# Performance work log

Measured on AMD Instinct MI355X. Metric: run time of the kernel, lower is better.

Reference implementation:

```python
import jax, jax.numpy as jnp
import numpy as np

V, E, H, S, B, T = 32000, 256, 512, 128, 32, 32


def setup_inputs() -> dict:
    key = jax.random.key(0)
    ks = iter(jax.random.split(key, 32))

    def w(shape, s=0.05):
        return jax.random.normal(next(ks), shape, dtype=jnp.float32) * s

    return dict(
        src=jax.random.randint(next(ks), (S, B), 0, V),
        trg=jax.random.randint(next(ks), (T, B), 0, V),
        embed=w((V, E)),
        enc_Wih_f=w((4 * H, E)), enc_Whh_f=w((4 * H, H)), enc_bih_f=w((4 * H,)), enc_bhh_f=w((4 * H,)),
        enc_Wih_b=w((4 * H, E)), enc_Whh_b=w((4 * H, H)), enc_bih_b=w((4 * H,)), enc_bhh_b=w((4 * H,)),
        attn_W=w((H, 2 * H)), attn_b=w((H,)), attn_v=w((H,)),
        dec_Wih0=w((4 * H, H + E)), dec_Whh0=w((4 * H, H)), dec_bih0=w((4 * H,)), dec_bhh0=w((4 * H,)),
        dec_Wih1=w((4 * H, H)), dec_Whh1=w((4 * H, H)), dec_bih1=w((4 * H,)), dec_bhh1=w((4 * H,)),
        out_W=w((V, 2 * H)), out_b=w((V,)),
    )


def _cell(x, h, c, Wih, Whh, bih, bhh):
    # PyTorch LSTM gate order: i, f, g, o
    z = x @ Wih.T + h @ Whh.T + bih + bhh
    i, f, g, o = jnp.split(z, 4, axis=-1)
    c2 = jax.nn.sigmoid(f) * c + jax.nn.sigmoid(i) * jnp.tanh(g)
    h2 = jax.nn.sigmoid(o) * jnp.tanh(c2)
    return h2, c2


def _run_lstm(xs, Wih, Whh, bih, bhh):
    # xs: [S, B, in]; returns outputs [S,B,H], final (h,c)
    h0 = jnp.zeros((xs.shape[1], Whh.shape[1]), xs.dtype)

    def step(carry, x):
        h, c = carry
        h2, c2 = _cell(x, h, c, Wih, Whh, bih, bhh)
        return (h2, c2), h2

    (hT, cT), outs = jax.lax.scan(step, (h0, h0), xs)
    return outs, hT, cT


def _forward(src, trg, embed,
             enc_Wih_f, enc_Whh_f, enc_bih_f, enc_bhh_f,
             enc_Wih_b, enc_Whh_b, enc_bih_b, enc_bhh_b,
             attn_W, attn_b, attn_v,
             dec_Wih0, dec_Whh0, dec_bih0, dec_bhh0,
             dec_Wih1, dec_Whh1, dec_bih1, dec_bhh1,
             out_W, out_b):
    emb_src = embed[src]                                  # [S,B,E]
    # bidirectional 1-layer encoder LSTM
    f_outs, hf, cf = _run_lstm(emb_src, enc_Wih_f, enc_Whh_f, enc_bih_f, enc_bhh_f)
    b_outs, hb, cb = _run_lstm(emb_src[::-1], enc_Wih_b, enc_Whh_b, enc_bih_b, enc_bhh_b)
    enc_out = f_outs + b_outs[::-1]                       # [S,B,H] (sum of directions)
    h = jnp.stack([hf, hb])                               # [2,B,H] -> decoder init state
    c = jnp.stack([cf, cb])
    enc_bsh = enc_out.transpose(1, 0, 2)                  # [B,S,H]

    def dec_step(carry, tok):
        h, c = carry
        emb = embed[tok]                                  # [B,E]
        q = h[-1]                                         # top-layer hidden [B,H]
        qs = jnp.broadcast_to(q[:, None, :], enc_bsh.shape)
        energy = jnp.tanh(jnp.concatenate([qs, enc_bsh], -1) @ attn_W.T + attn_b)  # [B,S,H]
        scores = energy @ attn_v                          # [B,S]
        aw = jax.nn.softmax(scores, axis=1)
        ctx = jnp.einsum('bs,bsh->bh', aw, enc_bsh)       # [B,H]
        x = jnp.concatenate([emb, ctx], -1)               # [B,E+H]
        h0, c0 = _cell(x, h[0], c[0], dec_Wih0, dec_Whh0, dec_bih0, dec_bhh0)
        h1, c1 = _cell(h0, h[1], c[1], dec_Wih1, dec_Whh1, dec_bih1, dec_bhh1)
        logits = jax.nn.log_softmax(
            jnp.concatenate([h1, ctx], -1) @ out_W.T + out_b, axis=-1)             # [B,V]
        return (jnp.stack([h0, h1]), jnp.stack([c0, c1])), logits

    # teacher forcing (ratio=1.0): input at step t is trg[t-1]
    _, outs = jax.lax.scan(dec_step, (h, c), trg[:-1])    # [T-1,B,V]
    outputs = jnp.concatenate(
        [jnp.zeros((1,) + outs.shape[1:], outs.dtype), outs], 0)  # outputs[0]=0 as in torch
    return outputs


def reference(src, trg, embed,
              enc_Wih_f, enc_Whh_f, enc_bih_f, enc_bhh_f,
              enc_Wih_b, enc_Whh_b, enc_bih_b, enc_bhh_b,
              attn_W, attn_b, attn_v,
              dec_Wih0, dec_Whh0, dec_bih0, dec_bhh0,
              dec_Wih1, dec_Whh1, dec_bih1, dec_bhh1,
              out_W, out_b):
    return _forward(src, trg, embed,
                    enc_Wih_f, enc_Whh_f, enc_bih_f, enc_bhh_f,
                    enc_Wih_b, enc_Whh_b, enc_bih_b, enc_bhh_b,
                    attn_W, attn_b, attn_v,
                    dec_Wih0, dec_Whh0, dec_bih0, dec_bhh0,
                    dec_Wih1, dec_Whh1, dec_bih1, dec_bhh1,
                    out_W, out_b)
```

## Files before the change

### kernel.cpp

```cpp
#include <hip/hip_runtime.h>
#include <stdint.h>


using short8 = __attribute__((ext_vector_type(8))) short;
using f32x4  = __attribute__((ext_vector_type(4))) float;
typedef _Float16 half2v __attribute__((ext_vector_type(2)));

__device__ __forceinline__ short f2bf(float x){
  unsigned u = __float_as_uint(x);
  unsigned r = (u + 0x7fffu + ((u >> 16) & 1u)) >> 16;
  return (short)(unsigned short)r;
}
__device__ __forceinline__ float bf2f_lo(unsigned u){ return __uint_as_float(u << 16); }
__device__ __forceinline__ float bf2f_hi(unsigned u){ return __uint_as_float(u & 0xffff0000u); }
__device__ __forceinline__ float sigmf(float x){ return 1.0f/(1.0f + __expf(-x)); }
__device__ __forceinline__ float fast_tanh(float x){
  const float e = __expf(2.0f*x);
  return 1.0f - 2.0f/(e + 1.0f);
}
__device__ __forceinline__ unsigned pack_h2(float a, float b){
  unsigned short ha = __builtin_bit_cast(unsigned short, (_Float16)a);
  unsigned short hb = __builtin_bit_cast(unsigned short, (_Float16)b);
  return (unsigned)ha | ((unsigned)hb << 16);
}
__device__ __forceinline__ float h2lo(unsigned u){ return (float)__builtin_bit_cast(half2v,u)[0]; }
__device__ __forceinline__ float h2hi(unsigned u){ return (float)__builtin_bit_cast(half2v,u)[1]; }
__device__ __forceinline__ float dot2u(unsigned x, unsigned w, float c){
#if __has_builtin(__builtin_amdgcn_fdot2)
  return __builtin_amdgcn_fdot2(__builtin_bit_cast(half2v,x), __builtin_bit_cast(half2v,w), c, false);
#else
  half2v hx = __builtin_bit_cast(half2v,x), hw = __builtin_bit_cast(half2v,w);
  c = fmaf((float)hx[0], (float)hw[0], c);
  c = fmaf((float)hx[1], (float)hw[1], c);
  return c;
#endif
}

__device__ __forceinline__ float4 load_coh_f4(const float* p){
  float4 v;
  asm volatile("global_load_dwordx4 %0, %1, off sc0 sc1\n\ts_waitcnt vmcnt(0)"
               : "=&v"(v) : "v"(p) : "memory");
  return v;
}
__device__ __forceinline__ void store_coh_u32(unsigned* p, unsigned v){
  asm volatile("global_store_dword %0, %1, off sc0 sc1" :: "v"(p), "v"(v) : "memory");
}

__device__ __forceinline__ void wait_spread(const unsigned* base, int n, unsigned target){
  if (threadIdx.x < 64){
    const bool mine = (int)threadIdx.x < n;
    const unsigned* p = base + (threadIdx.x << 4);
    for(;;){
      unsigned v = target;
      if (mine)
        asm volatile("global_load_dword %0, %1, off sc0 sc1\n\ts_waitcnt vmcnt(0)"
                     : "=&v"(v) : "v"(p) : "memory");
      if (__all(v >= target)) break;
    }
  }
  __syncthreads();
}
__device__ __forceinline__ void set_flag_sp(unsigned* slot, unsigned val){
  asm volatile("s_waitcnt vmcnt(0)" ::: "memory");
  __syncthreads();
  if (threadIdx.x == 0) store_coh_u32(slot, val);
}

__device__ __forceinline__ void stage8u(const unsigned* src, int bg, unsigned* lds){
  const unsigned* s0 = src + (size_t)bg*2048;
  const int f0 = threadIdx.x, f1 = f0 + 256;
  uint4 a, b;
  asm volatile(
    "global_load_dwordx4 %0, %2, off sc0 sc1\n\t"
    "global_load_dwordx4 %1, %3, off sc0 sc1\n\t"
    "s_waitcnt vmcnt(0)"
    : "=&v"(a), "=&v"(b)
    : "v"(s0 + (f0<<2)), "v"(s0 + (f1<<2))
    : "memory");
  { const int row = f0>>6, cu = (f0&63)<<2; *(uint4*)&lds[row*260+cu] = a; }
  { const int row = f1>>6, cu = (f1&63)<<2; *(uint4*)&lds[row*260+cu] = b; }
}

__device__ __forceinline__ float dot512(const unsigned* xrow, const unsigned* w){
  float a = 0.f;
  #pragma unroll 4
  for (int it = 0; it < 16; ++it){
    uint4 x0 = *(const uint4*)(xrow + it*16);
    uint4 x1 = *(const uint4*)(xrow + it*16 + 4);
    uint4 x2 = *(const uint4*)(xrow + it*16 + 8);
    uint4 x3 = *(const uint4*)(xrow + it*16 + 12);
    uint4 w0 = *(const uint4*)(w + it*16);
    uint4 w1 = *(const uint4*)(w + it*16 + 4);
    uint4 w2 = *(const uint4*)(w + it*16 + 8);
    uint4 w3 = *(const uint4*)(w + it*16 + 12);
    a = dot2u(x0.x,w0.x,a); a = dot2u(x0.y,w0.y,a); a = dot2u(x0.z,w0.z,a); a = dot2u(x0.w,w0.w,a);
    a = dot2u(x1.x,w1.x,a); a = dot2u(x1.y,w1.y,a); a = dot2u(x1.z,w1.z,a); a = dot2u(x1.w,w1.w,a);
    a = dot2u(x2.x,w2.x,a); a = dot2u(x2.y,w2.y,a); a = dot2u(x2.z,w2.z,a); a = dot2u(x2.w,w2.w,a);
    a = dot2u(x3.x,w3.x,a); a = dot2u(x3.y,w3.y,a); a = dot2u(x3.z,w3.z,a); a = dot2u(x3.w,w3.w,a);
  }
  return a;
}

__device__ __forceinline__ float2 dot2rows(const unsigned* xrow, const unsigned* wA, const unsigned* wB){
  float a = 0.f, b = 0.f;
  #pragma unroll 8
  for (int it = 0; it < 32; ++it){
    uint4 x0 = *(const uint4*)(xrow + it*8);
    uint4 x1 = *(const uint4*)(xrow + it*8 + 4);
    uint4 a0 = *(const uint4*)(wA + it*8);
    uint4 a1 = *(const uint4*)(wA + it*8 + 4);
    uint4 b0 = *(const uint4*)(wB + it*8);
    uint4 b1 = *(const uint4*)(wB + it*8 + 4);
    a = dot2u(x0.x,a0.x,a); a = dot2u(x0.y,a0.y,a); a = dot2u(x0.z,a0.z,a); a = dot2u(x0.w,a0.w,a);
    a = dot2u(x1.x,a1.x,a); a = dot2u(x1.y,a1.y,a); a = dot2u(x1.z,a1.z,a); a = dot2u(x1.w,a1.w,a);
    b = dot2u(x0.x,b0.x,b); b = dot2u(x0.y,b0.y,b); b = dot2u(x0.z,b0.z,b); b = dot2u(x0.w,b0.w,b);
    b = dot2u(x1.x,b1.x,b); b = dot2u(x1.y,b1.y,b); b = dot2u(x1.z,b1.z,b); b = dot2u(x1.w,b1.w,b);
  }
  return make_float2(a, b);
}

__global__ void k_zero(float* __restrict__ p, int n){
  int i = blockIdx.x*256 + threadIdx.x;
  const int stride = gridDim.x*256;
  for (; i < n; i += stride) p[i] = 0.f;
}

__global__ __launch_bounds__(256) void k_cvt_f16(const float* __restrict__ s, unsigned short* __restrict__ d, int n){
  int i = blockIdx.x*256 + threadIdx.x;
  const int stride = gridDim.x*256;
  for (; i < n; i += stride) d[i] = __builtin_bit_cast(unsigned short, (_Float16)s[i]);
}
__global__ __launch_bounds__(256) void k_cvt_f16_str(const float* __restrict__ s, int lds_, unsigned short* __restrict__ d, int n){
  int i = blockIdx.x*256 + threadIdx.x;
  const int stride = gridDim.x*256;
  for (; i < n; i += stride){
    const int row = i >> 9, c = i & 511;
    d[i] = __builtin_bit_cast(unsigned short, (_Float16)s[(size_t)row*lds_ + c]);
  }
}

__global__ __launch_bounds__(256) void k_gather(
    const int* __restrict__ src, const int* __restrict__ trg,
    const float* __restrict__ embed,
    short* __restrict__ emb_src_bf, short* __restrict__ emb_trg_bf)
{
  const int row = blockIdx.x, tid = threadIdx.x;
  if (row < 4096){
    const int tok = src[row];
    emb_src_bf[(size_t)row*256 + tid] = f2bf(embed[(size_t)tok*256 + tid]);
  } else {
    const int r = row - 4096;
    short v = 0;
    if (r < 992){ const int tok = trg[r]; v = f2bf(embed[(size_t)tok*256 + tid]); }
    emb_trg_bf[(size_t)r*256 + tid] = v;
  }
}

__global__ __launch_bounds__(256) void k_gemm_aw(
    const short* __restrict__ A, int lda,
    const float* __restrict__ W, int ldw,
    float* __restrict__ C, int ldc,
    const float* __restrict__ bias0, const float* __restrict__ bias1,
    int Mvalid, int K, int tmode, short* __restrict__ Cbf)
{
  __shared__ __align__(16) short As[128*32];
  __shared__ __align__(16) short Bs[128*32];
  const int tid = threadIdx.x;
  const int bm = blockIdx.x, bn = blockIdx.y;
  const int w  = tid >> 6,  l  = tid & 63;
  const int wm = w >> 1,    wn = w & 1;
  const int lr = l & 15,    lk = l >> 4;

  const int r0 = tid >> 2;
  const int s0 = (tid & 3) << 3;
  const int r1 = r0 + 64;

  const short* a0 = A + (size_t)(bm*128 + r0)*lda + s0;
  const short* a1 = A + (size_t)(bm*128 + r1)*lda + s0;
  const float* w0 = W + (size_t)(bn*128 + r0)*ldw + s0;
  const float* w1 = W + (size_t)(bn*128 + r1)*ldw + s0;

  const f32x4 zero4 = {0.f,0.f,0.f,0.f};
  f32x4 acc[4][4];
  #pragma unroll
  for (int mi=0;mi<4;mi++){
    #pragma unroll
    for (int ni=0;ni<4;ni++) acc[mi][ni] = zero4;
  }

  for (int k0 = 0; k0 < K; k0 += 32){
    short8 va0 = *(const short8*)(a0 + k0);
    short8 va1 = *(const short8*)(a1 + k0);
    float4 f00 = *(const float4*)(w0 + k0);
    float4 f01 = *(const float4*)(w0 + k0 + 4);
    float4 f10 = *(const float4*)(w1 + k0);
    float4 f11 = *(const float4*)(w1 + k0 + 4);
    short8 vb0, vb1;
    vb0[0]=f2bf(f00.x); vb0[1]=f2bf(f00.y); vb0[2]=f2bf(f00.z); vb0[3]=f2bf(f00.w);
    vb0[4]=f2bf(f01.x); vb0[5]=f2bf(f01.y); vb0[6]=f2bf(f01.z); vb0[7]=f2bf(f01.w);
    vb1[0]=f2bf(f10.x); vb1[1]=f2bf(f10.y); vb1[2]=f2bf(f10.z); vb1[3]=f2bf(f10.w);
    vb1[4]=f2bf(f11.x); vb1[5]=f2bf(f11.y); vb1[6]=f2bf(f11.z); vb1[7]=f2bf(f11.w);

    __syncthreads();
    *((short8*)As + tid)       = va0;
    *((short8*)As + tid + 256) = va1;
    *((short8*)Bs + tid)       = vb0;
    *((short8*)Bs + tid + 256) = vb1;
    __syncthreads();

    short8 af[4], bfr[4];
    #pragma unroll
    for (int mi=0;mi<4;mi++) af[mi]  = *(const short8*)&As[(wm*64 + mi*16 + lr)*32 + (lk<<3)];
    #pragma unroll
    for (int ni=0;ni<4;ni++) bfr[ni] = *(const short8*)&Bs[(wn*64 + ni*16 + lr)*32 + (lk<<3)];
    #pragma unroll
    for (int mi=0;mi<4;mi++){
      #pragma unroll
      for (int ni=0;ni<4;ni++)
        acc[mi][ni] = __builtin_amdgcn_mfma_f32_16x16x32_bf16(af[mi], bfr[ni], acc[mi][ni], 0,0,0);
    }
  }

  #pragma unroll
  for (int mi=0;mi<4;mi++){
    const int rb = bm*128 + wm*64 + mi*16 + (lk<<2);
    #pragma unroll
    for (int ni=0;ni<4;ni++){
      const int col = bn*128 + wn*64 + ni*16 + lr;
      float bv = 0.f;
      if (bias0) bv += bias0[col];
      if (bias1) bv += bias1[col];
      #pragma unroll
      for (int rr=0;rr<4;rr++){
        const int row = rb + rr;
        if (row < Mvalid){
          const float vv = acc[mi][ni][rr] + bv;
          if (Cbf)        Cbf[(size_t)row*ldc + col] = f2bf(vv);
          else if (tmode) C[(size_t)(row>>5)*65536 + (size_t)col*32 + (row&31)] = vv;
          else            C[(size_t)row*ldc + col] = vv;
        }
      }
    }
  }
}

__global__ __launch_bounds__(256,1) void k_enc_persist(
    const float* __restrict__ pre_f, const float* __restrict__ pre_b,
    const unsigned short* __restrict__ WhF, const unsigned short* __restrict__ WhB,
    unsigned* __restrict__ f_outs, unsigned* __restrict__ b_outs,
    float* __restrict__ c_f_out, float* __restrict__ c_b_out,
    unsigned* __restrict__ eflag)
{
  __shared__ __align__(16) unsigned x_lds[8*260];
  __shared__ float zbuf[64*8];
  const int bid = blockIdx.x, tid = threadIdx.x;
  const int x = bid & 7, m = bid >> 3;
  const int dir = m & 1, bg = (m >> 1) & 3, q = m >> 3;
  const int jb = x*4 + q;
  const float* pre = dir ? pre_b : pre_f;
  const unsigned* Wh = (const unsigned*)(dir ? WhB : WhF);
  unsigned* outs = dir ? b_outs : f_outs;
  float* c_out = dir ? c_b_out : c_f_out;
  unsigned* flags = eflag + (size_t)(dir*4 + bg)*512;

  const int bb = tid & 7, rr = tid >> 3;
  const int g = rr >> 3, op = rr & 7;
  const unsigned* wA = Wh + (size_t)(g*512 + jb*16 + 2*op)*256;
  const unsigned* wB = wA + 256;

  const int fo = tid & 15, fb = tid >> 4;
  const int b_out = bg*8 + fb, k_out = jb*16 + fo;
  float c_reg = 0.f;

  for (int t = 0; t < 128; ++t){
    float pz[4];
    if (tid < 128){
      const int tt = dir ? (127 - t) : t;
      const float* pt = pre + (size_t)tt*65536;
      #pragma unroll
      for (int gg = 0; gg < 4; ++gg)
        pz[gg] = pt[(size_t)(gg*512 + k_out)*32 + b_out];
    }
    if (t){
      wait_spread(flags, 32, (unsigned)t);
      stage8u(outs + (size_t)(t-1)*8192, bg, x_lds);
    } else {
      for (int i = tid; i < 8*260; i += 256) x_lds[i] = 0;
    }
    __syncthreads();

    const float2 d = dot2rows(x_lds + bb*260, wA, wB);
    zbuf[(g*16 + 2*op)*8 + bb]   = d.x;
    zbuf[(g*16 + 2*op+1)*8 + bb] = d.y;
    __syncthreads();

    if (tid < 128){
      float z[4];
      #pragma unroll
      for (int gg = 0; gg < 4; ++gg)
        z[gg] = pz[gg] + zbuf[(gg*16 + fo)*8 + fb];
      const float cn = sigmf(z[1])*c_reg + sigmf(z[0])*fast_tanh(z[2]);
      c_reg = cn;
      const float hn = sigmf(z[3])*fast_tanh(cn);
      const unsigned pu = pack_h2(hn, __shfl_xor(hn, 1));
      if (!(tid & 1))
        store_coh_u32(outs + (size_t)t*8192 + (size_t)b_out*256 + (k_out>>1), pu);
    }
    set_flag_sp(flags + jb*16, (unsigned)(t+1));
  }
  if (tid < 128) c_out[b_out*512 + k_out] = c_reg;
}

__global__ __launch_bounds__(256) void k_sum_enc(
    const unsigned* __restrict__ f_o, const unsigned* __restrict__ b_o,
    unsigned* __restrict__ enc_sum_bf_u)
{
  const int i = blockIdx.x*256 + threadIdx.x;
  const int s = i >> 13, rem = i & 8191;
  const unsigned a = f_o[i], b = b_o[(size_t)(127 - s)*8192 + rem];
  const float lo = h2lo(a) + h2lo(b);
  const float hi = h2hi(a) + h2hi(b);
  enc_sum_bf_u[i] = (unsigned)(unsigned short)f2bf(lo) | ((unsigned)(unsigned short)f2bf(hi) << 16);
}

__global__ __launch_bounds__(256,1) void k_dec_persist(
    const float* __restrict__ demb,
    const unsigned short* __restrict__ Wih0h,
    const unsigned short* __restrict__ Whh0h,
    const unsigned short* __restrict__ Wih1h,
    const unsigned short* __restrict__ Whh1h,
    const float* __restrict__ bih1, const float* __restrict__ bhh1,
    const unsigned short* __restrict__ wqh,
    const float* __restrict__ attnV,
    const short* __restrict__ enc_proj_bf,
    const short* __restrict__ enc_sum_bf,
    const unsigned* __restrict__ h0i, const unsigned* __restrict__ h1i,
    const float* __restrict__ c0_init, const float* __restrict__ c1_init,
    unsigned* __restrict__ h0buf, unsigned* __restrict__ h1buf,
    unsigned* __restrict__ ctxb,
    short* __restrict__ h1ctx,
    unsigned* __restrict__ flagC, unsigned* __restrict__ flagA)
{
  __shared__ __align__(16) unsigned x0s[8*260];
  __shared__ __align__(16) unsigned x1s[8*260];
  __shared__ float zfin[32*9];
  __shared__ __align__(16) float q_s[512], v_s[512];
  __shared__ float part[256], aw[128], red[128];

  const int bid = blockIdx.x, tid = threadIdx.x;
  const int jb = (bid & 7)*8 + ((bid >> 3) >> 2);
  const int bg = (bid >> 3) & 3;
  unsigned* grpC = flagC + bg*1024;
  unsigned* myC  = grpC + jb*16;
  unsigned* grpA = flagA + bg*128;

  const int b = tid & 7, r = tid >> 3;
  const int g = r >> 3, o = r & 7;
  const int j_row = g*512 + jb*8 + o;

  const int fo = tid & 7, fb = tid >> 3;
  const int b_out = bg*8 + fb, k_out = jb*8 + fo;

  const unsigned* Wh0row = (const unsigned*)Whh0h + (size_t)j_row*256;
  const unsigned* Wh1row = (const unsigned*)Whh1h + (size_t)j_row*256;
  const unsigned* Wi0row = (const unsigned*)Wih0h + (size_t)j_row*256;
  const unsigned* Wi1row = (const unsigned*)Wih1h + (size_t)j_row*256;
  const unsigned* WQ     = (const unsigned*)wqh;

  float c0_reg = 0.f, c1_reg = 0.f, bias1g[4];
  if (tid < 64){
    c0_reg = c0_init[b_out*512 + k_out];
    c1_reg = c1_init[b_out*512 + k_out];
    #pragma unroll
    for (int gg=0; gg<4; ++gg) bias1g[gg] = bih1[gg*512 + k_out] + bhh1[gg*512 + k_out];
  }
  if (bid < 32 && tid < 128) ((float4*)v_s)[tid] = ((const float4*)attnV)[tid];

  float zh0 = 0.f;

  for (int t = 0; t < 31; ++t){
    const float demb_v = demb[(size_t)t*65536 + (size_t)j_row*32 + bg*8 + b];

    if (t){
      wait_spread(grpC, 64, (unsigned)(2*t));
      stage8u(h1buf + (size_t)(t&1)*8192, bg, x1s);
    } else {
      stage8u(h1i, bg, x1s);
      stage8u(h0i, bg, x0s);
    }
    __syncthreads();
    if (t == 0) zh0 = dot512(x0s + b*260, Wh0row);
    if (bid < 32){
      const int ab = bid;
      {
        const float2 qq = dot2rows(x1s + (ab&7)*260,
                                   WQ + (size_t)tid*256, WQ + (size_t)(tid+256)*256);
        q_s[tid] = qq.x; q_s[tid+256] = qq.y;
      }
      __syncthreads();
      {
        const int s = tid >> 1, half = tid & 1;
        const unsigned* ep = (const unsigned*)(enc_proj_bf + ((size_t)(s*32 + ab))*512 + (half << 8));
        const float* qh = q_s + (half << 8);
        const float* vh = v_s + (half << 8);
        float p = 0.f;
        for (int kk = 0; kk < 128; kk += 4){
          uint4 e = *(const uint4*)(ep + kk);
          const int k2 = kk << 1;
          p += fast_tanh(qh[k2+0] + bf2f_lo(e.x)) * vh[k2+0];
          p += fast_tanh(qh[k2+1] + bf2f_hi(e.x)) * vh[k2+1];
          p += fast_tanh(qh[k2+2] + bf2f_lo(e.y)) * vh[k2+2];
          p += fast_tanh(qh[k2+3] + bf2f_hi(e.y)) * vh[k2+3];
          p += fast_tanh(qh[k2+4] + bf2f_lo(e.z)) * vh[k2+4];
          p += fast_tanh(qh[k2+5] + bf2f_hi(e.z)) * vh[k2+5];
          p += fast_tanh(qh[k2+6] + bf2f_lo(e.w)) * vh[k2+6];
          p += fast_tanh(qh[k2+7] + bf2f_hi(e.w)) * vh[k2+7];
        }
        part[tid] = p;
      }
      __syncthreads();
      if (tid < 128){ const float sc = part[2*tid] + part[2*tid+1]; aw[tid] = sc; red[tid] = sc; }
      __syncthreads();
      for (int off = 64; off > 0; off >>= 1){
        if (tid < off) red[tid] = fmaxf(red[tid], red[tid+off]);
        __syncthreads();
      }
      const float mx = red[0];
      __syncthreads();
      if (tid < 128){ const float e = __expf(aw[tid] - mx); aw[tid] = e; red[tid] = e; }
      __syncthreads();
      for (int off = 64; off > 0; off >>= 1){
        if (tid < off) red[tid] += red[tid+off];
        __syncthreads();
      }
      const float inv = 1.0f / red[0];
      if (tid < 128) aw[tid] *= inv;
      __syncthreads();
      {
        const int cc = tid << 1;
        float x0 = 0.f, x1 = 0.f;
        for (int s2 = 0; s2 < 128; ++s2){
          const unsigned u = *(const unsigned*)(enc_sum_bf + ((size_t)(s2*32 + ab))*512 + cc);
          const float a = aw[s2];
          x0 = fmaf(a, bf2f_lo(u), x0);
          x1 = fmaf(a, bf2f_hi(u), x1);
        }
        store_coh_u32(ctxb + (size_t)ab*256 + tid, pack_h2(x0, x1));
        h1ctx[(size_t)t*32768 + ab*1024 + 512 + cc]     = f2bf(x0);
        h1ctx[(size_t)t*32768 + ab*1024 + 512 + cc + 1] = f2bf(x1);
      }
      set_flag_sp(grpA + (bid&7)*16, (unsigned)(t+1));
    }

    wait_spread(grpA, 8, (unsigned)(t+1));
    const float zh1 = dot512(x1s + b*260, Wh1row);
    stage8u(ctxb, bg, x0s);
    __syncthreads();
    zfin[r*9 + b] = demb_v + dot512(x0s + b*260, Wi0row) + zh0;
    __syncthreads();
    if (tid < 64){
      float z[4];
      #pragma unroll
      for (int gg=0; gg<4; ++gg) z[gg] = zfin[(gg*8 + fo)*9 + fb];
      const float cn = sigmf(z[1])*c0_reg + sigmf(z[0])*fast_tanh(z[2]);
      c0_reg = cn;
      const float hn = sigmf(z[3])*fast_tanh(cn);
      const unsigned pu = pack_h2(hn, __shfl_xor(hn, 1));
      if (!(tid & 1))
        store_coh_u32(h0buf + (size_t)((t+1)&1)*8192 + (size_t)b_out*256 + (k_out>>1), pu);
    }
    set_flag_sp(myC, (unsigned)(2*t+1));

    wait_spread(grpC, 64, (unsigned)(2*t+1));
    stage8u(h0buf + (size_t)((t+1)&1)*8192, bg, x0s);
    __syncthreads();
    {
      const float2 d = dot2rows(x0s + b*260, Wi1row, Wh0row);
      zfin[r*9 + b] = d.x + zh1;
      zh0 = d.y;
    }
    __syncthreads();
    if (tid < 64){
      float z[4];
      #pragma unroll
      for (int gg=0; gg<4; ++gg) z[gg] = bias1g[gg] + zfin[(gg*8 + fo)*9 + fb];
      const float cn = sigmf(z[1])*c1_reg + sigmf(z[0])*fast_tanh(z[2]);
      c1_reg = cn;
      const float hn = sigmf(z[3])*fast_tanh(cn);
      const unsigned pu = pack_h2(hn, __shfl_xor(hn, 1));
      if (!(tid & 1))
        store_coh_u32(h1buf + (size_t)((t+1)&1)*8192 + (size_t)b_out*256 + (k_out>>1), pu);
      h1ctx[(size_t)t*32768 + (size_t)b_out*1024 + k_out] = f2bf(hn);
    }
    set_flag_sp(myC, (unsigned)(2*t+2));
  }
}

__global__ __launch_bounds__(256) void k_logsm(float* __restrict__ out){
  float* row = out + (size_t)blockIdx.x * 32000;
  const int tid = threadIdx.x;
  __shared__ float red[256];
  float s = 0.f;
  for (int i = tid; i < 8000; i += 256){
    const float4 v = ((const float4*)row)[i];
    s += __expf(v.x) + __expf(v.y) + __expf(v.z) + __expf(v.w);
  }
  red[tid] = s; __syncthreads();
  for (int off = 128; off > 0; off >>= 1){
    if (tid < off) red[tid] += red[tid+off];
    __syncthreads();
  }
  const float lse = __logf(red[0]);
  for (int i = tid; i < 8000; i += 256){
    float4 v = ((const float4*)row)[i];
    v.x -= lse; v.y -= lse; v.z -= lse; v.w -= lse;
    ((float4*)row)[i] = v;
  }
}

extern "C" void kernel_launch(void* const* d_in, const int* in_sizes, int n_in,
                              void* d_out, int out_size, void* d_ws, size_t ws_size,
                              hipStream_t stream)
{
  (void)in_sizes; (void)n_in; (void)out_size; (void)ws_size;
  const int*   src   = (const int*)d_in[0];
  const int*   trg   = (const int*)d_in[1];
  const float* embed = (const float*)d_in[2];
  const float* eWihF = (const float*)d_in[3];
  const float* eWhhF = (const float*)d_in[4];
  const float* ebihF = (const float*)d_in[5];
  const float* ebhhF = (const float*)d_in[6];
  const float* eWihB = (const float*)d_in[7];
  const float* eWhhB = (const float*)d_in[8];
  const float* ebihB = (const float*)d_in[9];
  const float* ebhhB = (const float*)d_in[10];
  const float* attnW = (const float*)d_in[11];
  const float* attnB = (const float*)d_in[12];
  const float* attnV = (const float*)d_in[13];
  const float* dWih0 = (const float*)d_in[14];
  const float* dWhh0 = (const float*)d_in[15];
  const float* dbih0 = (const float*)d_in[16];
  const float* dbhh0 = (const float*)d_in[17];
  const float* dWih1 = (const float*)d_in[18];
  const float* dWhh1 = (const float*)d_in[19];
  const float* dbih1 = (const float*)d_in[20];
  const float* dbhh1 = (const float*)d_in[21];
  const float* outW  = (const float*)d_in[22];
  const float* outB  = (const float*)d_in[23];

  float* out = (float*)d_out;
  float* enc_in_f = out;
  float* enc_in_b = out + 8388608;
  short* enc_proj_bf = (short*)(out + 18874368);
  unsigned* f_outs = (unsigned*)(out + 20971520);
  unsigned* b_outs = (unsigned*)(out + 23068672);
  float* demb     = out + 25165824;
  short* emb_src_bf = (short*)(out + 27262976);
  short* emb_trg_bf = (short*)(out + 27787264);
  unsigned* enc_sum_bf_u = (unsigned*)(out + 27918336);
  unsigned short* wqh    = (unsigned short*)(out + 28966912);
  unsigned short* whhF_h = (unsigned short*)(out + 29229056);
  unsigned short* whhB_h = (unsigned short*)(out + 29753344);
  unsigned short* wih0_h = (unsigned short*)(out + 30277632);
  unsigned short* whh0_h = (unsigned short*)(out + 30801920);
  unsigned short* wih1_h = (unsigned short*)(out + 31326208);
  unsigned short* whh1_h = (unsigned short*)(out + 31850496);

  char* ws = (char*)d_ws;
  short* h1ctx = (short*)ws;
  unsigned* h0buf = (unsigned*)(ws + 2097152);
  unsigned* h1buf = (unsigned*)(ws + 2162688);
  unsigned* ctxb  = (unsigned*)(ws + 2228224);
  float* c_f      = (float*)(ws + 2260992);
  float* c_b      = (float*)(ws + 2326528);
  unsigned* eflag = (unsigned*)(ws + 2392064);
  unsigned* flagC = (unsigned*)(ws + 2408448);
  unsigned* flagA = (unsigned*)(ws + 2424832);

  k_zero<<<4, 256, 0, stream>>>((float*)eflag, 8704);
  k_gather<<<5120, 256, 0, stream>>>(src, trg, embed, emb_src_bf, emb_trg_bf);
  {
    dim3 g1(32,16);
    k_gemm_aw<<<g1,256,0,stream>>>(emb_src_bf,256, eWihF,256, enc_in_f,2048, ebihF,ebhhF, 4096,256, 1, nullptr);
    k_gemm_aw<<<g1,256,0,stream>>>(emb_src_bf,256, eWihB,256, enc_in_b,2048, ebihB,ebhhB, 4096,256, 1, nullptr);
    dim3 g2(8,16);
    k_gemm_aw<<<g2,256,0,stream>>>(emb_trg_bf,256, dWih0,768, demb,2048, dbih0,dbhh0, 1024,256, 1, nullptr);
  }
  k_cvt_f16<<<1024,256,0,stream>>>(eWhhF, whhF_h, 1048576);
  k_cvt_f16<<<1024,256,0,stream>>>(eWhhB, whhB_h, 1048576);
  k_cvt_f16_str<<<1024,256,0,stream>>>(dWih0+256, 768, wih0_h, 1048576);
  k_cvt_f16<<<1024,256,0,stream>>>(dWhh0, whh0_h, 1048576);
  k_cvt_f16<<<1024,256,0,stream>>>(dWih1, wih1_h, 1048576);
  k_cvt_f16<<<1024,256,0,stream>>>(dWhh1, whh1_h, 1048576);
  k_cvt_f16_str<<<256,256,0,stream>>>(attnW, 1024, wqh, 262144);
  k_enc_persist<<<256, 256, 0, stream>>>(enc_in_f, enc_in_b, whhF_h, whhB_h,
                                         f_outs, b_outs, c_f, c_b, eflag);
  k_sum_enc<<<4096, 256, 0, stream>>>(f_outs, b_outs, enc_sum_bf_u);
  {
    dim3 g3(32,4);
    k_gemm_aw<<<g3,256,0,stream>>>((const short*)enc_sum_bf_u,512, attnW+512,1024, nullptr,512, attnB,nullptr, 4096,512, 0, enc_proj_bf);
  }
  k_dec_persist<<<256, 256, 0, stream>>>(demb, wih0_h, whh0_h, wih1_h, whh1_h,
                                         dbih1, dbhh1, wqh, attnV, enc_proj_bf,
                                         (const short*)enc_sum_bf_u,
                                         f_outs + (size_t)127*8192, b_outs + (size_t)127*8192,
                                         c_f, c_b, h0buf, h1buf, ctxb, h1ctx, flagC, flagA);
  k_zero<<<512, 256, 0, stream>>>(out, 1024000);
  {
    dim3 g4(8,250);
    k_gemm_aw<<<g4,256,0,stream>>>(h1ctx,1024, outW,1024, out + 1024000, 32000, outB,nullptr, 992,1024, 0, nullptr);
  }
  k_logsm<<<992, 256, 0, stream>>>(out + 1024000);
}
```

Baseline: 2.705 ms.

## Repartition decoder persistent kernel into 8 batch groups and distribute query projection

```diff
diff --git a/kernel.cpp b/kernel.cpp
--- a/kernel.cpp
+++ b/kernel.cpp
@@ -42,7 +42,16 @@
                : "=&v"(v) : "v"(p) : "memory");
   return v;
 }
+__device__ __forceinline__ uint4 load_coh_u4(const unsigned* p){
+  uint4 v;
+  asm volatile("global_load_dwordx4 %0, %1, off sc0 sc1\n\ts_waitcnt vmcnt(0)"
+               : "=&v"(v) : "v"(p) : "memory");
+  return v;
+}
 __device__ __forceinline__ void store_coh_u32(unsigned* p, unsigned v){
+  asm volatile("global_store_dword %0, %1, off sc0 sc1" :: "v"(p), "v"(v) : "memory");
+}
+__device__ __forceinline__ void store_coh_f32(float* p, float v){
   asm volatile("global_store_dword %0, %1, off sc0 sc1" :: "v"(p), "v"(v) : "memory");
 }
 
@@ -66,8 +75,8 @@
   if (threadIdx.x == 0) store_coh_u32(slot, val);
 }
 
-__device__ __forceinline__ void stage8u(const unsigned* src, int bg, unsigned* lds){
-  const unsigned* s0 = src + (size_t)bg*2048;
+__device__ __forceinline__ void stage8u(const unsigned* src, int bg8, unsigned* lds){
+  const unsigned* s0 = src + (size_t)bg8*2048;
   const int f0 = threadIdx.x, f1 = f0 + 256;
   uint4 a, b;
   asm volatile(
@@ -79,6 +88,16 @@
     : "memory");
   { const int row = f0>>6, cu = (f0&63)<<2; *(uint4*)&lds[row*260+cu] = a; }
   { const int row = f1>>6, cu = (f1&63)<<2; *(uint4*)&lds[row*260+cu] = b; }
+}
+
+__device__ __forceinline__ void stage4u(const unsigned* src, int bg4, unsigned* lds){
+  const unsigned* s0 = src + (size_t)bg4*1024;
+  uint4 a;
+  asm volatile(
+    "global_load_dwordx4 %0, %1, off sc0 sc1\n\ts_waitcnt vmcnt(0)"
+    : "=&v"(a) : "v"(s0 + (threadIdx.x<<2)) : "memory");
+  const int row = threadIdx.x>>6, cu = (threadIdx.x&63)<<2;
+  *(uint4*)&lds[row*260+cu] = a;
 }
 
 __device__ __forceinline__ float dot512(const unsigned* xrow, const unsigned* w){
@@ -333,39 +352,48 @@
     const unsigned short* __restrict__ wqh,
     const float* __restrict__ attnV,
     const short* __restrict__ enc_proj_bf,
-    const short* __restrict__ enc_sum_bf,
+    const unsigned* __restrict__ enc_sum_u,
     const unsigned* __restrict__ h0i, const unsigned* __restrict__ h1i,
     const float* __restrict__ c0_init, const float* __restrict__ c1_init,
     unsigned* __restrict__ h0buf, unsigned* __restrict__ h1buf,
     unsigned* __restrict__ ctxb,
+    float* __restrict__ qsb,
     short* __restrict__ h1ctx,
-    unsigned* __restrict__ flagC, unsigned* __restrict__ flagA)
+    unsigned* __restrict__ flagQ, unsigned* __restrict__ flagH0,
+    unsigned* __restrict__ flagH1, unsigned* __restrict__ flagCtx)
 {
-  __shared__ __align__(16) unsigned x0s[8*260];
-  __shared__ __align__(16) unsigned x1s[8*260];
-  __shared__ float zfin[32*9];
+  __shared__ __align__(16) unsigned x1s[4*260];
+  __shared__ __align__(16) unsigned x0s[4*260];
+  __shared__ float zfin[64*5];
   __shared__ __align__(16) float q_s[512], v_s[512];
   __shared__ float part[256], aw[128], red[128];
 
   const int bid = blockIdx.x, tid = threadIdx.x;
-  const int jb = (bid & 7)*8 + ((bid >> 3) >> 2);
-  const int bg = (bid >> 3) & 3;
-  unsigned* grpC = flagC + bg*1024;
-  unsigned* myC  = grpC + jb*16;
-  unsigned* grpA = flagA + bg*128;
-
-  const int b = tid & 7, r = tid >> 3;
-  const int g = r >> 3, o = r & 7;
-  const int j_row = g*512 + jb*8 + o;
-
-  const int fo = tid & 7, fb = tid >> 3;
-  const int b_out = bg*8 + fb, k_out = jb*8 + fo;
+  const int x = bid & 7, m = bid >> 3;
+  const int bg = m & 7, q = m >> 3;
+  const int jb = x*4 + q;
+  const bool is_attn = ((jb & 7) == 0);
+  const int ar = jb >> 3;
+  const int ab = bg*4 + ar;
+
+  unsigned* fQ  = flagQ  + bg*512;
+  unsigned* fH0 = flagH0 + bg*512;
+  unsigned* fH1 = flagH1 + bg*512;
+  unsigned* fCt = flagCtx + bg*64;
+
+  const int b  = tid & 3;
+  const int jr = tid >> 2;
+  const int g  = jr >> 4, col = jr & 15;
+  const int j_row = g*512 + jb*16 + col;
+
+  const int fcol = tid & 15, fb2 = tid >> 4;
+  const int b_out = bg*4 + fb2, k_out = jb*16 + fcol;
 
   const unsigned* Wh0row = (const unsigned*)Whh0h + (size_t)j_row*256;
   const unsigned* Wh1row = (const unsigned*)Whh1h + (size_t)j_row*256;
   const unsigned* Wi0row = (const unsigned*)Wih0h + (size_t)j_row*256;
   const unsigned* Wi1row = (const unsigned*)Wih1h + (size_t)j_row*256;
-  const unsigned* WQ     = (const unsigned*)wqh;
+  const unsigned* WQu    = (const unsigned*)wqh;
 
   float c0_reg = 0.f, c1_reg = 0.f, bias1g[4];
   if (tid < 64){
@@ -374,29 +402,33 @@
     #pragma unroll
     for (int gg=0; gg<4; ++gg) bias1g[gg] = bih1[gg*512 + k_out] + bhh1[gg*512 + k_out];
   }
-  if (bid < 32 && tid < 128) ((float4*)v_s)[tid] = ((const float4*)attnV)[tid];
+  if (is_attn && tid < 128) ((float4*)v_s)[tid] = ((const float4*)attnV)[tid];
 
   float zh0 = 0.f;
 
   for (int t = 0; t < 31; ++t){
-    const float demb_v = demb[(size_t)t*65536 + (size_t)j_row*32 + bg*8 + b];
+    const float demb_v = demb[(size_t)t*65536 + (size_t)j_row*32 + bg*4 + b];
 
     if (t){
-      wait_spread(grpC, 64, (unsigned)(2*t));
-      stage8u(h1buf + (size_t)(t&1)*8192, bg, x1s);
+      wait_spread(fH1, 32, (unsigned)t);
+      stage4u(h1buf + (size_t)(t&1)*8192, bg, x1s);
     } else {
-      stage8u(h1i, bg, x1s);
-      stage8u(h0i, bg, x0s);
+      stage4u(h1i, bg, x1s);
+      stage4u(h0i, bg, x0s);
     }
     __syncthreads();
     if (t == 0) zh0 = dot512(x0s + b*260, Wh0row);
-    if (bid < 32){
-      const int ab = bid;
-      {
-        const float2 qq = dot2rows(x1s + (ab&7)*260,
-                                   WQ + (size_t)tid*256, WQ + (size_t)(tid+256)*256);
-        q_s[tid] = qq.x; q_s[tid+256] = qq.y;
-      }
+    const float zh1 = dot512(x1s + b*260, Wh1row);
+    if (tid < 64){
+      const int qb = tid >> 4, qcol = jb*16 + (tid & 15);
+      const float qv = dot512(x1s + qb*260, WQu + (size_t)qcol*256);
+      store_coh_f32(qsb + (size_t)(bg*4 + qb)*512 + qcol, qv);
+    }
+    set_flag_sp(fQ + jb*16, (unsigned)(t+1));
+
+    if (is_attn){
+      wait_spread(fQ, 32, (unsigned)(t+1));
+      if (tid < 128) ((float4*)q_s)[tid] = load_coh_f4(qsb + (size_t)ab*512 + (tid<<2));
       __syncthreads();
       {
         const int s = tid >> 1, half = tid & 1;
@@ -440,7 +472,7 @@
         const int cc = tid << 1;
         float x0 = 0.f, x1 = 0.f;
         for (int s2 = 0; s2 < 128; ++s2){
-          const unsigned u = *(const unsigned*)(enc_sum_bf + ((size_t)(s2*32 + ab))*512 + cc);
+          const unsigned u = enc_sum_u[(size_t)(s2*32 + ab)*256 + tid];
           const float a = aw[s2];
           x0 = fmaf(a, bf2f_lo(u), x0);
           x1 = fmaf(a, bf2f_hi(u), x1);
@@ -449,19 +481,18 @@
         h1ctx[(size_t)t*32768 + ab*1024 + 512 + cc]     = f2bf(x0);
         h1ctx[(size_t)t*32768 + ab*1024 + 512 + cc + 1] = f2bf(x1);
       }
-      set_flag_sp(grpA + (bid&7)*16, (unsigned)(t+1));
-    }
-
-    wait_spread(grpA, 8, (unsigned)(t+1));
-    const float zh1 = dot512(x1s + b*260, Wh1row);
-    stage8u(ctxb, bg, x0s);
-    __syncthreads();
-    zfin[r*9 + b] = demb_v + dot512(x0s + b*260, Wi0row) + zh0;
+      set_flag_sp(fCt + ar*16, (unsigned)(t+1));
+    }
+
+    wait_spread(fCt, 4, (unsigned)(t+1));
+    stage4u(ctxb, bg, x0s);
+    __syncthreads();
+    zfin[jr*5 + b] = demb_v + dot512(x0s + b*260, Wi0row) + zh0;
     __syncthreads();
     if (tid < 64){
       float z[4];
       #pragma unroll
-      for (int gg=0; gg<4; ++gg) z[gg] = zfin[(gg*8 + fo)*9 + fb];
+      for (int gg=0; gg<4; ++gg) z[gg] = zfin[(gg*16 + fcol)*5 + fb2];
       const float cn = sigmf(z[1])*c0_reg + sigmf(z[0])*fast_tanh(z[2]);
       c0_reg = cn;
       const float hn = sigmf(z[3])*fast_tanh(cn);
@@ -469,21 +500,21 @@
       if (!(tid & 1))
         store_coh_u32(h0buf + (size_t)((t+1)&1)*8192 + (size_t)b_out*256 + (k_out>>1), pu);
     }
-    set_flag_sp(myC, (unsigned)(2*t+1));
-
-    wait_spread(grpC, 64, (unsigned)(2*t+1));
-    stage8u(h0buf + (size_t)((t+1)&1)*8192, bg, x0s);
+    set_flag_sp(fH0 + jb*16, (unsigned)(t+1));
+
+    wait_spread(fH0, 32, (unsigned)(t+1));
+    stage4u(h0buf + (size_t)((t+1)&1)*8192, bg, x1s);
     __syncthreads();
     {
-      const float2 d = dot2rows(x0s + b*260, Wi1row, Wh0row);
-      zfin[r*9 + b] = d.x + zh1;
+      const float2 d = dot2rows(x1s + b*260, Wi1row, Wh0row);
+      zfin[jr*5 + b] = d.x + zh1;
       zh0 = d.y;
     }
     __syncthreads();
     if (tid < 64){
       float z[4];
       #pragma unroll
-      for (int gg=0; gg<4; ++gg) z[gg] = bias1g[gg] + zfin[(gg*8 + fo)*9 + fb];
+      for (int gg=0; gg<4; ++gg) z[gg] = bias1g[gg] + zfin[(gg*16 + fcol)*5 + fb2];
       const float cn = sigmf(z[1])*c1_reg + sigmf(z[0])*fast_tanh(z[2]);
       c1_reg = cn;
       const float hn = sigmf(z[3])*fast_tanh(cn);
@@ -492,7 +523,7 @@
         store_coh_u32(h1buf + (size_t)((t+1)&1)*8192 + (size_t)b_out*256 + (k_out>>1), pu);
       h1ctx[(size_t)t*32768 + (size_t)b_out*1024 + k_out] = f2bf(hn);
     }
-    set_flag_sp(myC, (unsigned)(2*t+2));
+    set_flag_sp(fH1 + jb*16, (unsigned)(t+1));
   }
 }
 
@@ -565,6 +596,7 @@
   unsigned short* whh0_h = (unsigned short*)(out + 30801920);
   unsigned short* wih1_h = (unsigned short*)(out + 31326208);
   unsigned short* whh1_h = (unsigned short*)(out + 31850496);
+  float* qsb            = out + 32374784;
 
   char* ws = (char*)d_ws;
   short* h1ctx = (short*)ws;
@@ -573,11 +605,13 @@
   unsigned* ctxb  = (unsigned*)(ws + 2228224);
   float* c_f      = (float*)(ws + 2260992);
   float* c_b      = (float*)(ws + 2326528);
-  unsigned* eflag = (unsigned*)(ws + 2392064);
-  unsigned* flagC = (unsigned*)(ws + 2408448);
-  unsigned* flagA = (unsigned*)(ws + 2424832);
-
-  k_zero<<<4, 256, 0, stream>>>((float*)eflag, 8704);
+  unsigned* eflag   = (unsigned*)(ws + 2392064);
+  unsigned* flagQ   = (unsigned*)(ws + 2408448);
+  unsigned* flagH0  = (unsigned*)(ws + 2424832);
+  unsigned* flagH1  = (unsigned*)(ws + 2441216);
+  unsigned* flagCtx = (unsigned*)(ws + 2457600);
+
+  k_zero<<<8, 256, 0, stream>>>((float*)eflag, 16896);
   k_gather<<<5120, 256, 0, stream>>>(src, trg, embed, emb_src_bf, emb_trg_bf);
   {
     dim3 g1(32,16);
@@ -602,9 +636,10 @@
   }
   k_dec_persist<<<256, 256, 0, stream>>>(demb, wih0_h, whh0_h, wih1_h, whh1_h,
                                          dbih1, dbhh1, wqh, attnV, enc_proj_bf,
-                                         (const short*)enc_sum_bf_u,
+                                         enc_sum_bf_u,
                                          f_outs + (size_t)127*8192, b_outs + (size_t)127*8192,
-                                         c_f, c_b, h0buf, h1buf, ctxb, h1ctx, flagC, flagA);
+                                         c_f, c_b, h0buf, h1buf, ctxb, qsb, h1ctx,
+                                         flagQ, flagH0, flagH1, flagCtx);
   k_zero<<<512, 256, 0, stream>>>(out, 1024000);
   {
     dim3 g4(8,250);
```

New measurement: 2.410 ms. 10.9% less time.
